# Kernel tuning notes

Hardware: AMD Instinct MI355X
Metric: run time of the kernel (lower is better)

## Reference

```python
import jax, jax.numpy as jnp
import numpy as np

T, B, C, H = 2048, 4, 1024, 16
DK = C // H
CLAMP = 1e8  # fp32 clamp bound used by the original module


def setup_inputs() -> dict:
    key = jax.random.key(0)
    ks = jax.random.split(key, 12)
    s = 1.0 / np.sqrt(C)
    inp = {
        'query': jax.random.normal(ks[0], (T, B, C), jnp.float32),
        'key': jax.random.normal(ks[1], (T, B, C), jnp.float32),
        'value': jax.random.normal(ks[2], (T, B, C), jnp.float32),
        'key_padding_mask': jax.random.randint(ks[3], (B, T), 0, 2) > 0,
        # nn.Linear params, stored torch-style as [out, in]
        'Wq': jax.random.uniform(ks[4], (C, C), jnp.float32, -s, s),
        'bq': jax.random.uniform(ks[5], (C,), jnp.float32, -s, s),
        'Wk': jax.random.uniform(ks[6], (C, C), jnp.float32, -s, s),
        'bk': jax.random.uniform(ks[7], (C,), jnp.float32, -s, s),
        'Wv': jax.random.uniform(ks[8], (C, C), jnp.float32, -s, s),
        'bv': jax.random.uniform(ks[9], (C,), jnp.float32, -s, s),
        'Wo': jax.random.uniform(ks[10], (C, C), jnp.float32, -s, s),
        'bo': jax.random.uniform(ks[11], (C,), jnp.float32, -s, s),
    }
    return inp


def _attn(query, key, value, key_padding_mask, Wq, bq, Wk, bk, Wv, bv, Wo, bo):
    # T x B x C -> B x T x C
    q_in = jnp.swapaxes(query, 0, 1)
    k_in = jnp.swapaxes(key, 0, 1)
    v_in = jnp.swapaxes(value, 0, 1)
    b = q_in.shape[0]
    # projections (torch Linear: x @ W.T + b), split heads -> B x H x T x dk
    q = (q_in @ Wq.T + bq).reshape(b, -1, H, DK).transpose(0, 2, 1, 3)
    k = (k_in @ Wk.T + bk).reshape(b, -1, H, DK).transpose(0, 2, 1, 3)
    v = (v_in @ Wv.T + bv).reshape(b, -1, H, DK).transpose(0, 2, 1, 3)
    scores = jnp.einsum('bhqd,bhkd->bhqk', q, k) / np.sqrt(DK)
    if key_padding_mask is not None:
        scores = jnp.where(key_padding_mask[:, None, None, :], -jnp.inf, scores)
    scores = jnp.clip(scores, -CLAMP, CLAMP)
    attn = jax.nn.softmax(scores.astype(jnp.float32), axis=-1).astype(scores.dtype)
    # dropout is identity in eval mode
    x = jnp.einsum('bhqk,bhkd->bhqd', attn, v)
    x = x.transpose(0, 2, 1, 3).reshape(b, -1, H * DK)
    out = x @ Wo.T + bo
    return jnp.swapaxes(out, 0, 1)  # back to T x B x C


def reference(query, key, value, key_padding_mask, Wq, bq, Wk, bk, Wv, bv, Wo, bo):
    return _attn(query, key, value, key_padding_mask, Wq, bq, Wk, bk, Wv, bv, Wo, bo)
```

## Files before the change

### kernel.cpp

```cpp
#include <hip/hip_runtime.h>
#include <hip/hip_bf16.h>
#include <cstddef>
#include <cstdint>

constexpr int T  = 2048;
constexpr int B  = 4;
constexpr int C  = 1024;
constexpr int H  = 16;
constexpr int DK = 64;
constexpr int M  = T * B;
constexpr int NT = T / 64;

typedef __attribute__((ext_vector_type(8))) short bf16x8;
typedef __attribute__((ext_vector_type(4))) float f32x4;
typedef __attribute__((ext_vector_type(4))) unsigned short u16x4;
typedef __attribute__((ext_vector_type(8))) unsigned short u16x8;

__device__ inline unsigned short f2bf(float f) {
    union { float f; uint32_t u; } v; v.f = f;
    uint32_t u = v.u + 0x7fff + ((v.u >> 16) & 1);
    return (unsigned short)(u >> 16);
}
__device__ inline float bf2f(unsigned short h) {
    union { uint32_t u; float f; } v; v.u = (uint32_t)h << 16;
    return v.f;
}
__device__ inline uint32_t cvtpk_bf16(float lo, float hi) {
    uint32_t r;
    asm("v_cvt_pk_bf16_f32 %0, %1, %2" : "=v"(r) : "v"(lo), "v"(hi));
    return r;
}
__device__ inline void cfence() { asm volatile("" ::: "memory"); }

__device__ inline void block_sync_lds() {
    __builtin_amdgcn_sched_barrier(0);
    asm volatile("s_waitcnt lgkmcnt(0)" ::: "memory");
    __builtin_amdgcn_sched_barrier(0);
    __builtin_amdgcn_s_barrier();
    __builtin_amdgcn_sched_barrier(0);
}

__device__ inline void gload_lds16(const void* g, void* l) {
    auto gp = reinterpret_cast<const __attribute__((address_space(1))) char*>(
        reinterpret_cast<uintptr_t>(g));
    auto lp = reinterpret_cast<__attribute__((address_space(3))) char*>(
        reinterpret_cast<uintptr_t>(l));
    __builtin_amdgcn_global_load_lds(gp, lp, 16, 0, 0);
}

__global__ __launch_bounds__(256) void convert_in(const float* __restrict__ q,
                                                  const float* __restrict__ k,
                                                  const float* __restrict__ v,
                                                  unsigned short* __restrict__ dq,
                                                  unsigned short* __restrict__ dk2,
                                                  unsigned short* __restrict__ dv) {
    const float* s; unsigned short* d;
    if (blockIdx.y == 0) { s = q; d = dq; }
    else if (blockIdx.y == 1) { s = k; d = dk2; }
    else { s = v; d = dv; }
    const size_t i = ((size_t)blockIdx.x * 256 + threadIdx.x) * 8;
    const float4 a = *(const float4*)(s + i);
    const float4 b = *(const float4*)(s + i + 4);
    u16x8 o;
    o[0] = f2bf(a.x); o[1] = f2bf(a.y); o[2] = f2bf(a.z); o[3] = f2bf(a.w);
    o[4] = f2bf(b.x); o[5] = f2bf(b.y); o[6] = f2bf(b.z); o[7] = f2bf(b.w);
    *(u16x8*)(d + i) = o;
}

__global__ __launch_bounds__(256) void convert_w(const float* __restrict__ wq,
                                                 const float* __restrict__ wk,
                                                 const float* __restrict__ wv,
                                                 unsigned short* __restrict__ dst) {
    const float* s = blockIdx.y == 0 ? wq : (blockIdx.y == 1 ? wk : wv);
    unsigned short* d = dst + (size_t)blockIdx.y * C * C;
    const size_t i = ((size_t)blockIdx.x * 256 + threadIdx.x) * 8;
    const float4 a = *(const float4*)(s + i);
    const float4 b = *(const float4*)(s + i + 4);
    u16x8 o;
    o[0] = f2bf(a.x); o[1] = f2bf(a.y); o[2] = f2bf(a.z); o[3] = f2bf(a.w);
    o[4] = f2bf(b.x); o[5] = f2bf(b.y); o[6] = f2bf(b.z); o[7] = f2bf(b.w);
    *(u16x8*)(d + i) = o;
}

__global__ __launch_bounds__(256) void convert_wo(const float* __restrict__ wo,
                                                  unsigned short* __restrict__ hi,
                                                  unsigned short* __restrict__ lo) {
    const size_t i = ((size_t)blockIdx.x * 256 + threadIdx.x) * 8;
#pragma unroll
    for (int j = 0; j < 8; j++) {
        const float x = wo[i + j];
        const unsigned short h = f2bf(x);
        hi[i + j] = h;
        lo[i + j] = f2bf(x - bf2f(h));
    }
}

__global__ __launch_bounds__(256) void qkv_gemm(
        const unsigned short* __restrict__ Aq,
        const unsigned short* __restrict__ Ak,
        const unsigned short* __restrict__ Av,
        const unsigned short* __restrict__ W,
        const float* __restrict__ bq, const float* __restrict__ bk,
        const float* __restrict__ bv,
        unsigned short* __restrict__ Qb, unsigned short* __restrict__ Kb,
        unsigned short* __restrict__ Vb) {
    __shared__ __align__(16) unsigned short As[128][32];
    __shared__ __align__(16) unsigned short Ws[128][32];

    const int tid = threadIdx.x;
    const int m0 = blockIdx.x * 128;
    const int n0 = blockIdx.y * 128;
    const int w = tid >> 6, lane = tid & 63;
    const int g = lane >> 4, c16 = lane & 15;
    const int wr = (w >> 1) * 64, wc = (w & 1) * 64;

    const int which = n0 >> 10;
    const unsigned short* A = which == 0 ? Aq : (which == 1 ? Ak : Av);

    f32x4 acc[4][4] = {};

    for (int k0 = 0; k0 < C; k0 += 32) {
        __syncthreads();
#pragma unroll
        for (int half = 0; half < 2; half++) {
            const int chunk = tid + half * 256;
            const int r = chunk >> 2, s = chunk & 3;
            gload_lds16(A + (size_t)(m0 + r) * C + k0 + s * 8,
                        (char*)&As[0][0] + chunk * 16);
            gload_lds16(W + (size_t)(n0 + r) * C + k0 + s * 8,
                        (char*)&Ws[0][0] + chunk * 16);
        }
        __syncthreads();

        bf16x8 af[4], bfr[4];
#pragma unroll
        for (int mf = 0; mf < 4; mf++)
            af[mf] = *(const bf16x8*)&As[wr + mf * 16 + c16][g * 8];
#pragma unroll
        for (int nf = 0; nf < 4; nf++)
            bfr[nf] = *(const bf16x8*)&Ws[wc + nf * 16 + c16][g * 8];
#pragma unroll
        for (int mf = 0; mf < 4; mf++)
#pragma unroll
            for (int nf = 0; nf < 4; nf++)
                acc[mf][nf] = __builtin_amdgcn_mfma_f32_16x16x32_bf16(
                    af[mf], bfr[nf], acc[mf][nf], 0, 0, 0);
    }

    unsigned short* dst = which == 0 ? Qb : (which == 1 ? Kb : Vb);
    const float* bias = which == 0 ? bq : (which == 1 ? bk : bv);
    const float scale = which == 0 ? 0.180336889f : 1.0f;

#pragma unroll
    for (int mf = 0; mf < 4; mf++) {
#pragma unroll
        for (int nf = 0; nf < 4; nf++) {
            const int n = n0 + wc + nf * 16 + c16;
            const int c = n & 1023;
            const int hh = c >> 6, dk = c & 63;
            const float bval = bias[c];
#pragma unroll
            for (int r = 0; r < 4; r++) {
                const int m = m0 + wr + mf * 16 + g * 4 + r;
                const int t = m >> 2, bb = m & 3;
                dst[((size_t)(bb * H + hh) * T + t) * DK + dk] =
                    f2bf((acc[mf][nf][r] + bval) * scale);
            }
        }
    }
}

__global__ __launch_bounds__(256) void oproj_gemm(
        const unsigned short* __restrict__ Xh, const unsigned short* __restrict__ Xl,
        const unsigned short* __restrict__ Wh, const unsigned short* __restrict__ Wl,
        const float* __restrict__ bo, float* __restrict__ out) {
    __shared__ __align__(16) unsigned short Ahs[128][32];
    __shared__ __align__(16) unsigned short Als[128][32];
    __shared__ __align__(16) unsigned short Bhs[128][32];
    __shared__ __align__(16) unsigned short Bls[128][32];

    const int tid = threadIdx.x;
    const int m0 = blockIdx.x * 128;
    const int n0 = blockIdx.y * 128;
    const int w = tid >> 6, lane = tid & 63;
    const int g = lane >> 4, c16 = lane & 15;
    const int wr = (w >> 1) * 64, wc = (w & 1) * 64;

    f32x4 acc[4][4] = {};

    for (int k0 = 0; k0 < C; k0 += 32) {
        __syncthreads();
#pragma unroll
        for (int half = 0; half < 2; half++) {
            const int chunk = tid + half * 256;
            const int r = chunk >> 2, s = chunk & 3;
            const size_t goffA = (size_t)(m0 + r) * C + k0 + s * 8;
            const size_t goffB = (size_t)(n0 + r) * C + k0 + s * 8;
            gload_lds16(Xh + goffA, (char*)&Ahs[0][0] + chunk * 16);
            gload_lds16(Xl + goffA, (char*)&Als[0][0] + chunk * 16);
            gload_lds16(Wh + goffB, (char*)&Bhs[0][0] + chunk * 16);
            gload_lds16(Wl + goffB, (char*)&Bls[0][0] + chunk * 16);
        }
        __syncthreads();

        bf16x8 ah[4], al[4];
#pragma unroll
        for (int mf = 0; mf < 4; mf++) {
            ah[mf] = *(const bf16x8*)&Ahs[wr + mf * 16 + c16][g * 8];
            al[mf] = *(const bf16x8*)&Als[wr + mf * 16 + c16][g * 8];
        }
#pragma unroll
        for (int nf = 0; nf < 4; nf++) {
            const bf16x8 wh = *(const bf16x8*)&Bhs[wc + nf * 16 + c16][g * 8];
            const bf16x8 wl = *(const bf16x8*)&Bls[wc + nf * 16 + c16][g * 8];
#pragma unroll
            for (int mf = 0; mf < 4; mf++) {
                acc[mf][nf] = __builtin_amdgcn_mfma_f32_16x16x32_bf16(ah[mf], wh, acc[mf][nf], 0, 0, 0);
                acc[mf][nf] = __builtin_amdgcn_mfma_f32_16x16x32_bf16(al[mf], wh, acc[mf][nf], 0, 0, 0);
                acc[mf][nf] = __builtin_amdgcn_mfma_f32_16x16x32_bf16(ah[mf], wl, acc[mf][nf], 0, 0, 0);
            }
        }
    }

#pragma unroll
    for (int mf = 0; mf < 4; mf++) {
#pragma unroll
        for (int nf = 0; nf < 4; nf++) {
            const int n = n0 + wc + nf * 16 + c16;
            const float bval = bo[n];
#pragma unroll
            for (int r = 0; r < 4; r++) {
                const int m = m0 + wr + mf * 16 + g * 4 + r;
                const int t = m & 2047, bb = m >> 11;
                out[((size_t)t * B + bb) * C + n] = acc[mf][nf][r] + bval;
            }
        }
    }
}

__global__ __launch_bounds__(256) void attn_mfma(const unsigned short* __restrict__ Q,
                                                 const unsigned short* __restrict__ K,
                                                 const unsigned short* __restrict__ V,
                                                 const int* __restrict__ mask,
                                                 unsigned short* __restrict__ Xh,
                                                 unsigned short* __restrict__ Xl) {
    __shared__ __align__(16) short Ks[2][64][72];
    __shared__ __align__(16) short Vt[2][64][72];
    __shared__ __align__(16) short Pl[4][16][72];

    const int b = blockIdx.z, h = blockIdx.y;
    const int q0 = blockIdx.x * 128;
    const int tid = threadIdx.x;
    const int wl = tid >> 6;
    const int lane = tid & 63;
    const int g = lane >> 4;
    const int c16 = lane & 15;

    const size_t bh = (size_t)(b * H + h) * T * DK;
    const unsigned short* Qg = Q + bh;
    const unsigned short* Kg = K + bh;
    const unsigned short* Vg = V + bh;
    const int* mb = mask + b * T;

    bf16x8 qf[2][2];
#pragma unroll
    for (int qs = 0; qs < 2; qs++)
#pragma unroll
        for (int sl = 0; sl < 2; sl++)
            qf[qs][sl] = *(const bf16x8*)(Qg +
                (size_t)(q0 + wl * 32 + qs * 16 + c16) * DK + g * 8 + sl * 32);

    f32x4 o[2][4] = {};
    float lrow[2] = {0.0f, 0.0f};

    const int skr = tid >> 3;
    const int skc = (tid & 7) * 8;
    const int kp = tid & 31, dc = tid >> 5;
    uint4 kra, krb; u16x8 va, vb; int mw;

#define ISSUE(kv0)                                                              \
    do {                                                                        \
        kra = *(const uint4*)(Kg + (size_t)((kv0) + skr) * DK + skc);           \
        krb = *(const uint4*)(Kg + (size_t)((kv0) + skr + 32) * DK + skc);      \
        va  = *(const u16x8*)(Vg + (size_t)((kv0) + 2 * kp) * DK + dc * 8);     \
        vb  = *(const u16x8*)(Vg + (size_t)((kv0) + 2 * kp + 1) * DK + dc * 8); \
        mw  = mb[(kv0) + lane];                                                 \
    } while (0)

    ISSUE(0);

    for (int kt = 0; kt < NT; ++kt) {
        const int buf = kt & 1;

        const unsigned long long mbits = __ballot(mw != 0);
        *(uint4*)&Ks[buf][skr][skc] = kra;
        *(uint4*)&Ks[buf][skr + 32][skc] = krb;
#pragma unroll
        for (int j = 0; j < 8; j++) {
            *(uint32_t*)&Vt[buf][dc * 8 + j][2 * kp] =
                (uint32_t)(unsigned short)va[j] | ((uint32_t)(unsigned short)vb[j] << 16);
        }
        if (kt + 1 < NT) ISSUE((kt + 1) * 64);

        block_sync_lds();

        bf16x8 kf[4][2], vf[4][2];
#pragma unroll
        for (int t = 0; t < 4; t++)
#pragma unroll
            for (int sl = 0; sl < 2; sl++) {
                kf[t][sl] = *(const bf16x8*)&Ks[buf][t * 16 + c16][g * 8 + sl * 32];
                vf[t][sl] = *(const bf16x8*)&Vt[buf][t * 16 + c16][g * 8 + sl * 32];
            }

#pragma unroll
        for (int qs = 0; qs < 2; qs++) {
            f32x4 s4[4];
#pragma unroll
            for (int t = 0; t < 4; t++) {
                f32x4 acc = {0.f, 0.f, 0.f, 0.f};
                acc = __builtin_amdgcn_mfma_f32_16x16x32_bf16(kf[t][0], qf[qs][0], acc, 0, 0, 0);
                acc = __builtin_amdgcn_mfma_f32_16x16x32_bf16(kf[t][1], qf[qs][1], acc, 0, 0, 0);
                s4[t] = acc;
            }

            float rs = 0.0f;
#pragma unroll
            for (int t = 0; t < 4; t++)
#pragma unroll
                for (int r = 0; r < 4; r++) {
                    float p = __builtin_amdgcn_exp2f(s4[t][r]);
                    const int key = 16 * t + 4 * g + r;
                    p = ((mbits >> key) & 1ull) ? 0.0f : p;
                    s4[t][r] = p;
                    rs += p;
                }
            rs += __shfl_xor(rs, 16);
            rs += __shfl_xor(rs, 32);
            lrow[qs] += rs;

            cfence();
#pragma unroll
            for (int t = 0; t < 4; t++)
#pragma unroll
                for (int rr = 0; rr < 2; rr++) {
                    const uint32_t wv = cvtpk_bf16(s4[t][2 * rr], s4[t][2 * rr + 1]);
                    *(uint32_t*)&Pl[wl][c16][16 * t + 4 * g + 2 * rr] = wv;
                }
            cfence();
            bf16x8 pa[2];
            pa[0] = *(const bf16x8*)&Pl[wl][c16][g * 8];
            pa[1] = *(const bf16x8*)&Pl[wl][c16][g * 8 + 32];
            cfence();

#pragma unroll
            for (int td = 0; td < 4; td++) {
                o[qs][td] = __builtin_amdgcn_mfma_f32_16x16x32_bf16(vf[td][0], pa[0], o[qs][td], 0, 0, 0);
                o[qs][td] = __builtin_amdgcn_mfma_f32_16x16x32_bf16(vf[td][1], pa[1], o[qs][td], 0, 0, 0);
            }
        }
    }
#undef ISSUE

#pragma unroll
    for (int qs = 0; qs < 2; qs++) {
        const float inv = 1.0f / lrow[qs];
        const int qq = q0 + wl * 32 + qs * 16 + c16;
#pragma unroll
        for (int td = 0; td < 4; td++) {
            u16x4 hi4, lo4;
#pragma unroll
            for (int r = 0; r < 4; r++) {
                const float val = o[qs][td][r] * inv;
                const unsigned short hv = f2bf(val);
                hi4[r] = hv;
                lo4[r] = f2bf(val - bf2f(hv));
            }
            const size_t idx = ((size_t)b * T + qq) * C + h * DK + td * 16 + 4 * g;
            *(u16x4*)(Xh + idx) = hi4;
            *(u16x4*)(Xl + idx) = lo4;
        }
    }
}

extern "C" void kernel_launch(void* const* d_in, const int* in_sizes, int n_in,
                              void* d_out, int out_size, void* d_ws, size_t ws_size,
                              hipStream_t stream) {
    const float* query = (const float*)d_in[0];
    const float* key   = (const float*)d_in[1];
    const float* value = (const float*)d_in[2];
    const int*   kpm   = (const int*)d_in[3];
    const float* Wq = (const float*)d_in[4];
    const float* bq = (const float*)d_in[5];
    const float* Wk = (const float*)d_in[6];
    const float* bk = (const float*)d_in[7];
    const float* Wv = (const float*)d_in[8];
    const float* bv = (const float*)d_in[9];
    const float* Wo = (const float*)d_in[10];
    const float* bo = (const float*)d_in[11];

    constexpr size_t MB = 1u << 20;
    char* w8 = (char*)d_ws;
    unsigned short* Qa  = (unsigned short*)(w8 + 0 * MB);
    unsigned short* Ka  = (unsigned short*)(w8 + 16 * MB);
    unsigned short* Va  = (unsigned short*)(w8 + 32 * MB);
    unsigned short* WB  = (unsigned short*)(w8 + 48 * MB);
    unsigned short* WoH = (unsigned short*)(w8 + 54 * MB);
    unsigned short* WoL = (unsigned short*)(w8 + 56 * MB);
    unsigned short* Qb  = (unsigned short*)(w8 + 64 * MB);
    unsigned short* Kb  = (unsigned short*)(w8 + 80 * MB);
    unsigned short* Vb  = (unsigned short*)(w8 + 96 * MB);
    unsigned short* XhB = Qa;
    unsigned short* XlB = Ka;

    const dim3 blk(256);

    convert_in<<<dim3(4096, 3), blk, 0, stream>>>(query, key, value, Qa, Ka, Va);
    convert_w<<<dim3(512, 3), blk, 0, stream>>>(Wq, Wk, Wv, WB);
    convert_wo<<<dim3(512, 1), blk, 0, stream>>>(Wo, WoH, WoL);

    qkv_gemm<<<dim3(M / 128, 3 * C / 128), blk, 0, stream>>>(Qa, Ka, Va, WB,
                                                             bq, bk, bv,
                                                             Qb, Kb, Vb);

    attn_mfma<<<dim3(T / 128, H, B), blk, 0, stream>>>(Qb, Kb, Vb, kpm, XhB, XlB);

    oproj_gemm<<<dim3(M / 128, C / 128), blk, 0, stream>>>(XhB, XlB, WoH, WoL,
                                                           bo, (float*)d_out);
}
```

Measured before the change: 273.1 us.

## Software-pipeline global loads in the QKV and output-projection GEMMs

The QKV GEMM now double-buffers its LDS tiles. The next K-slice is issued with direct global-to-LDS loads while MFMAs run on the current buffer, which cuts the loop to one barrier per iteration. The output-projection GEMM instead prefetches the next K-slice of its hi/lo bf16 operands into registers, then stores them to LDS after the barrier. Both changes aim to hide global-load latency behind matrix math. The cost is double the LDS in the QKV kernel and extra registers in the projection kernel, which could lower occupancy.

```diff
diff --git a/kernel.cpp b/kernel.cpp
--- a/kernel.cpp
+++ b/kernel.cpp
@@ -104,8 +104,8 @@
         const float* __restrict__ bv,
         unsigned short* __restrict__ Qb, unsigned short* __restrict__ Kb,
         unsigned short* __restrict__ Vb) {
-    __shared__ __align__(16) unsigned short As[128][32];
-    __shared__ __align__(16) unsigned short Ws[128][32];
+    __shared__ __align__(16) unsigned short As[2][128][32];
+    __shared__ __align__(16) unsigned short Ws[2][128][32];
 
     const int tid = threadIdx.x;
     const int m0 = blockIdx.x * 128;
@@ -117,28 +117,42 @@
     const int which = n0 >> 10;
     const unsigned short* A = which == 0 ? Aq : (which == 1 ? Ak : Av);
 
+    const int lr = tid >> 2, ls = tid & 3;
+
     f32x4 acc[4][4] = {};
 
-    for (int k0 = 0; k0 < C; k0 += 32) {
+#pragma unroll
+    for (int half = 0; half < 2; half++) {
+        const int chunk = tid + half * 256;
+        const int r = chunk >> 2, s = chunk & 3;
+        gload_lds16(A + (size_t)(m0 + r) * C + s * 8, (char*)&As[0][0][0] + chunk * 16);
+        gload_lds16(W + (size_t)(n0 + r) * C + s * 8, (char*)&Ws[0][0][0] + chunk * 16);
+    }
+
+    for (int kt = 0; kt < C / 32; kt++) {
+        const int buf = kt & 1;
         __syncthreads();
-#pragma unroll
-        for (int half = 0; half < 2; half++) {
-            const int chunk = tid + half * 256;
-            const int r = chunk >> 2, s = chunk & 3;
-            gload_lds16(A + (size_t)(m0 + r) * C + k0 + s * 8,
-                        (char*)&As[0][0] + chunk * 16);
-            gload_lds16(W + (size_t)(n0 + r) * C + k0 + s * 8,
-                        (char*)&Ws[0][0] + chunk * 16);
-        }
-        __syncthreads();
+        if (kt + 1 < C / 32) {
+            const int k0n = (kt + 1) * 32;
+#pragma unroll
+            for (int half = 0; half < 2; half++) {
+                const int chunk = tid + half * 256;
+                const int r = chunk >> 2, s = chunk & 3;
+                gload_lds16(A + (size_t)(m0 + r) * C + k0n + s * 8,
+                            (char*)&As[buf ^ 1][0][0] + chunk * 16);
+                gload_lds16(W + (size_t)(n0 + r) * C + k0n + s * 8,
+                            (char*)&Ws[buf ^ 1][0][0] + chunk * 16);
+            }
+            __builtin_amdgcn_sched_barrier(0);
+        }
 
         bf16x8 af[4], bfr[4];
 #pragma unroll
         for (int mf = 0; mf < 4; mf++)
-            af[mf] = *(const bf16x8*)&As[wr + mf * 16 + c16][g * 8];
+            af[mf] = *(const bf16x8*)&As[buf][wr + mf * 16 + c16][g * 8];
 #pragma unroll
         for (int nf = 0; nf < 4; nf++)
-            bfr[nf] = *(const bf16x8*)&Ws[wc + nf * 16 + c16][g * 8];
+            bfr[nf] = *(const bf16x8*)&Ws[buf][wc + nf * 16 + c16][g * 8];
 #pragma unroll
         for (int mf = 0; mf < 4; mf++)
 #pragma unroll
@@ -188,20 +202,37 @@
 
     f32x4 acc[4][4] = {};
 
-    for (int k0 = 0; k0 < C; k0 += 32) {
-        __syncthreads();
-#pragma unroll
-        for (int half = 0; half < 2; half++) {
-            const int chunk = tid + half * 256;
-            const int r = chunk >> 2, s = chunk & 3;
-            const size_t goffA = (size_t)(m0 + r) * C + k0 + s * 8;
-            const size_t goffB = (size_t)(n0 + r) * C + k0 + s * 8;
-            gload_lds16(Xh + goffA, (char*)&Ahs[0][0] + chunk * 16);
-            gload_lds16(Xl + goffA, (char*)&Als[0][0] + chunk * 16);
-            gload_lds16(Wh + goffB, (char*)&Bhs[0][0] + chunk * 16);
-            gload_lds16(Wl + goffB, (char*)&Bls[0][0] + chunk * 16);
-        }
-        __syncthreads();
+    uint4 rXh[2], rXl[2], rWh[2], rWl[2];
+#define OISSUE(K0)                                                         \
+    do {                                                                   \
+        _Pragma("unroll")                                                  \
+        for (int i = 0; i < 2; i++) {                                      \
+            const int c = tid + i * 256;                                   \
+            const int r = c >> 2, s = c & 3;                               \
+            const size_t goffA = (size_t)(m0 + r) * C + (K0) + s * 8;      \
+            const size_t goffB = (size_t)(n0 + r) * C + (K0) + s * 8;      \
+            rXh[i] = *(const uint4*)(Xh + goffA);                          \
+            rXl[i] = *(const uint4*)(Xl + goffA);                          \
+            rWh[i] = *(const uint4*)(Wh + goffB);                          \
+            rWl[i] = *(const uint4*)(Wl + goffB);                          \
+        }                                                                  \
+    } while (0)
+
+    OISSUE(0);
+
+    for (int kt = 0; kt < C / 32; kt++) {
+        block_sync_lds();
+#pragma unroll
+        for (int i = 0; i < 2; i++) {
+            const int c = tid + i * 256;
+            *(uint4*)((char*)&Ahs[0][0] + c * 16) = rXh[i];
+            *(uint4*)((char*)&Als[0][0] + c * 16) = rXl[i];
+            *(uint4*)((char*)&Bhs[0][0] + c * 16) = rWh[i];
+            *(uint4*)((char*)&Bls[0][0] + c * 16) = rWl[i];
+        }
+        if (kt + 1 < C / 32) OISSUE((kt + 1) * 32);
+
+        block_sync_lds();
 
         bf16x8 ah[4], al[4];
 #pragma unroll
@@ -221,6 +252,7 @@
             }
         }
     }
+#undef OISSUE
 
 #pragma unroll
     for (int mf = 0; mf < 4; mf++) {
```

Measured after the change: 384.0 us. 1.41x slower.
